# Kernel tuning notes

Hardware: AMD Instinct MI355X
Metric: run time of the kernel (lower is better)

## Reference

```python
import jax, jax.numpy as jnp
import numpy as np

TEMP = 10.0  # self.temp in the module


def _l2norm(x, eps):
    # matches torch cosine_similarity / F.normalize eps-clamped L2 normalization
    n = jnp.sqrt(jnp.sum(x * x, axis=-1, keepdims=True))
    return x / jnp.maximum(n, eps)


def setup_inputs() -> dict:
    key = jax.random.key(0)
    k1, k2, k3, k4 = jax.random.split(key, 4)
    b, n, k, q, t, c = 2, 5, 5, 75, 196, 384  # 5-way 5-shot, 15 queries/way, ViT-S tokens
    return {
        "feat_shot": jax.random.normal(k1, (b, n, k, t, c), jnp.float32),
        "feat_query": jax.random.normal(k2, (b, q, t, c), jnp.float32),
        "x_shot": jax.random.normal(k3, (b, n, k, c), jnp.float32),
        "x_query": jax.random.normal(k4, (b, q, c), jnp.float32),
    }


def reference(feat_shot, feat_query, x_shot, x_query):
    b, n, k, t, c = feat_shot.shape
    # --- token-level cosine similarity branch ---
    fq = _l2norm(feat_query, 1e-8)                      # [b,q,t,c]
    fs = _l2norm(feat_shot.reshape(b, n, k * t, c), 1e-8)  # [b,n,k*t,c]
    # cosine sim of every query token vs every shot token of each class
    sim = jnp.einsum('bqtc,bnsc->bqnts', fq, fs)        # [b,q,n,t,k*t]
    # topk(k=1) over shot tokens -> max; .mean(-1) over the size-1 topk dim is identity;
    # then mean over query tokens t
    logits = jnp.max(sim, axis=-1).mean(axis=-1)        # [b,q,n]
    # --- global-feature classifier branch ---
    proto = _l2norm(x_shot.mean(axis=-2), 1e-12)        # prototype mean over k shots: [b,n,c]
    xq = _l2norm(x_query, 1e-12)                        # [b,q,c]
    cls_logits = TEMP * jnp.einsum('bqc,bnc->bqn', xq, proto)  # [b,q,n]
    return (logits, cls_logits)
```

## Files before the change

### kernel.cpp

```cpp
#include <hip/hip_runtime.h>
#include <hip/hip_bf16.h>
#include <hip/hip_fp8.h>
#include <stdint.h>


typedef __attribute__((ext_vector_type(8))) int int8v;
typedef __attribute__((ext_vector_type(4))) float f32x4;

__device__ __forceinline__ unsigned enc_f(float f) {
    unsigned b = __float_as_uint(f);
    return (b & 0x80000000u) ? ~b : (b | 0x80000000u);
}
__device__ __forceinline__ float dec_f(unsigned u) {
    unsigned b = (u & 0x80000000u) ? (u & 0x7FFFFFFFu) : ~u;
    return __uint_as_float(b);
}

__device__ __forceinline__ unsigned pack4_fp8(float a, float b, float c, float d) {
    int r = __builtin_amdgcn_cvt_pk_fp8_f32(a, b, 0, false);
    r = __builtin_amdgcn_cvt_pk_fp8_f32(c, d, r, true);
    return (unsigned)r;
}

__global__ void prep_kernel(const float* __restrict__ feat_query,
                            const float* __restrict__ feat_shot,
                            const float* __restrict__ x_shot,
                            unsigned* __restrict__ fqn,
                            unsigned* __restrict__ fsnp,
                            float* __restrict__ proto,
                            unsigned* __restrict__ P) {
    const int blk  = blockIdx.x;
    const int tid  = threadIdx.x;
    const int lane = tid & 63;
    const int wv   = tid >> 6;

    if (blk < 2478) {
        const int tr  = blk * 16 + wv * 4 + (lane >> 4);
        const int l16 = lane & 15;
        if (tr >= 39640) return;

        const float* row;
        unsigned* o32;
        bool zero = false;
        if (tr < 29400) {
            row = feat_query + (size_t)tr * 384;
            o32 = fqn + (size_t)tr * 96;
        } else {
            const int sp = tr - 29400;
            const int bn = sp >> 10;
            const int s  = sp & 1023;
            o32 = fsnp + (size_t)sp * 96;
            row = feat_shot + ((size_t)bn * 980 + s) * 384;
            zero = (s >= 980);
        }
        if (zero) {
#pragma unroll
            for (int j = 0; j < 6; ++j) o32[l16 + 16 * j] = 0u;
            return;
        }
        const float4* rf4 = (const float4*)row;
        float4 v[6];
        float ss = 0.f;
#pragma unroll
        for (int j = 0; j < 6; ++j) {
            v[j] = rf4[l16 + 16 * j];
            ss += v[j].x * v[j].x + v[j].y * v[j].y + v[j].z * v[j].z + v[j].w * v[j].w;
        }
#pragma unroll
        for (int off = 1; off < 16; off <<= 1) ss += __shfl_xor(ss, off, 64);
        const float sc = 1.0f / fmaxf(sqrtf(ss), 1e-8f);
#pragma unroll
        for (int j = 0; j < 6; ++j)
            o32[l16 + 16 * j] = pack4_fp8(v[j].x * sc, v[j].y * sc, v[j].z * sc, v[j].w * sc);
    } else if (blk < 2481) {
        const int gw = (blk - 2478) * 4 + wv;
        if (gw >= 10) return;
        const float* base = x_shot + (size_t)gw * 5 * 384;
        float v[6];
        float ss = 0.f;
#pragma unroll
        for (int j = 0; j < 6; ++j) {
            float s = 0.f;
#pragma unroll
            for (int kk = 0; kk < 5; ++kk) s += base[kk * 384 + lane + 64 * j];
            s *= 0.2f;
            v[j] = s;
            ss += s * s;
        }
#pragma unroll
        for (int off = 1; off < 64; off <<= 1) ss += __shfl_xor(ss, off, 64);
        const float scale = 1.0f / fmaxf(sqrtf(ss), 1e-12f);
#pragma unroll
        for (int j = 0; j < 6; ++j) proto[(size_t)gw * 384 + lane + 64 * j] = v[j] * scale;
    } else {
        const int i = (blk - 2481) * 256 + tid;
        if (i < 147000) P[i] = 0u;
    }
}

__global__ __launch_bounds__(256, 2) void gemm_kernel(const uint8_t* __restrict__ fqn,
                                                      const uint8_t* __restrict__ fsnp,
                                                      unsigned* __restrict__ P) {
    __shared__ __align__(16) uint8_t Bl[2][12288];

    const int bid = blockIdx.x;
    const int mt  = bid % 58;
    const int g1  = bid / 58;
    const int sh  = g1 & 1;
    const int bc  = g1 >> 1;
    const int b   = bc / 5;
    const int m0  = mt * 256;

    const int tid  = threadIdx.x;
    const int lane = tid & 63;
    const int wv   = tid >> 6;
    const int l15  = lane & 15;
    const int hi   = lane >> 4;

    const uint8_t* Ag = fqn  + (size_t)b * 14700 * 384;
    const uint8_t* Bg = fsnp + ((size_t)bc * 1024 + sh * 512) * 384;

    int8v A[4][3];
#pragma unroll
    for (int mi = 0; mi < 4; ++mi) {
        int row = m0 + wv * 64 + mi * 16 + l15;
        row = row < 14700 ? row : 14699;
        const uint8_t* pa = Ag + (size_t)row * 384 + hi * 32;
#pragma unroll
        for (int ks = 0; ks < 3; ++ks) {
            const uint4 x = *(const uint4*)(pa + ks * 128);
            const uint4 y = *(const uint4*)(pa + ks * 128 + 16);
            A[mi][ks] = (int8v){(int)x.x, (int)x.y, (int)x.z, (int)x.w,
                                (int)y.x, (int)y.y, (int)y.z, (int)y.w};
        }
    }

    int src_off[3];
#pragma unroll
    for (int rr = 0; rr < 3; ++rr) {
        const int idx = rr * 256 + tid;
        const int col = idx / 24;
        const int gp  = idx - col * 24;
        const int g   = (gp & ~7) | ((gp & 7) ^ (col & 7));
        src_off[rr] = col * 384 + g * 16;
    }
    const int lds_base = tid * 16;

    uint4 nx0 = *(const uint4*)(Bg + src_off[0]);
    uint4 nx1 = *(const uint4*)(Bg + src_off[1]);
    uint4 nx2 = *(const uint4*)(Bg + src_off[2]);

    float rmax[4][4];
#pragma unroll
    for (int mi = 0; mi < 4; ++mi)
#pragma unroll
        for (int i = 0; i < 4; ++i) rmax[mi][i] = -3.0e38f;

    const int c0 = ((2 * hi + 0) ^ (l15 & 7)) * 16;
    const int c1 = ((2 * hi + 1) ^ (l15 & 7)) * 16;

    for (int it = 0; it < 16; ++it) {
        uint8_t* wbuf = Bl[it & 1];
        *(uint4*)(&wbuf[lds_base])        = nx0;
        *(uint4*)(&wbuf[lds_base + 4096]) = nx1;
        *(uint4*)(&wbuf[lds_base + 8192]) = nx2;
        __syncthreads();

        if (it + 1 < 16) {
            const uint8_t* src = Bg + (size_t)(it + 1) * 32 * 384;
            nx0 = *(const uint4*)(src + src_off[0]);
            nx1 = *(const uint4*)(src + src_off[1]);
            nx2 = *(const uint4*)(src + src_off[2]);
        }

        const uint8_t* buf = Bl[it & 1];
        f32x4 acc[4][2];
#pragma unroll
        for (int mi = 0; mi < 4; ++mi)
#pragma unroll
            for (int nf = 0; nf < 2; ++nf) acc[mi][nf] = (f32x4){0.f, 0.f, 0.f, 0.f};

#pragma unroll
        for (int ks = 0; ks < 3; ++ks) {
            int8v Bf[2];
#pragma unroll
            for (int nf = 0; nf < 2; ++nf) {
                const uint8_t* base = buf + (nf * 16 + l15) * 384 + ks * 128;
                const uint4 x = *(const uint4*)(base + c0);
                const uint4 y = *(const uint4*)(base + c1);
                Bf[nf] = (int8v){(int)x.x, (int)x.y, (int)x.z, (int)x.w,
                                 (int)y.x, (int)y.y, (int)y.z, (int)y.w};
            }
#pragma unroll
            for (int mi = 0; mi < 4; ++mi)
#pragma unroll
                for (int nf = 0; nf < 2; ++nf)
                    acc[mi][nf] = __builtin_amdgcn_mfma_scale_f32_16x16x128_f8f6f4(
                        A[mi][ks], Bf[nf], acc[mi][nf],
                        0, 0,
                        0, 0x7F7F7F7F,
                        0, 0x7F7F7F7F);
        }

#pragma unroll
        for (int nf = 0; nf < 2; ++nf) {
            if (sh * 512 + it * 32 + nf * 16 + l15 < 980) {
#pragma unroll
                for (int mi = 0; mi < 4; ++mi)
#pragma unroll
                    for (int i = 0; i < 4; ++i)
                        rmax[mi][i] = fmaxf(rmax[mi][i], acc[mi][nf][i]);
            }
        }
    }

#pragma unroll
    for (int mi = 0; mi < 4; ++mi)
#pragma unroll
        for (int i = 0; i < 4; ++i) {
            float v = rmax[mi][i];
#pragma unroll
            for (int off = 1; off < 16; off <<= 1) v = fmaxf(v, __shfl_xor(v, off, 64));
            if (l15 == 0) {
                const int row = m0 + wv * 64 + mi * 16 + hi * 4 + i;
                if (row < 14700)
                    atomicMax(&P[(size_t)bc * 14700 + row], enc_f(v));
            }
        }
}

__global__ void final_kernel(const unsigned* __restrict__ P,
                             const float* __restrict__ xq,
                             const float* __restrict__ proto,
                             float* __restrict__ out) {
    const int blk  = blockIdx.x;
    const int tid  = threadIdx.x;
    const int lane = tid & 63;
    const int wv   = tid >> 6;

    if (blk < 188) {
        const int gw = blk * 4 + wv;
        if (gw >= 750) return;
        const int n  = gw % 5;
        const int bq = gw / 5;
        const int b  = bq / 75;
        const int q  = bq % 75;
        const unsigned* row = P + (size_t)(b * 5 + n) * 14700 + q * 196;
        float s = 0.f;
        for (int t = lane; t < 196; t += 64) s += dec_f(row[t]);
#pragma unroll
        for (int off = 1; off < 64; off <<= 1) s += __shfl_xor(s, off, 64);
        if (lane == 0) out[gw] = s * (1.0f / 196.0f);
    } else {
        const int gw = (blk - 188) * 4 + wv;
        if (gw >= 150) return;
        const float* row = xq + (size_t)gw * 384;
        float u[6];
        float ss = 0.f;
#pragma unroll
        for (int j = 0; j < 6; ++j) { u[j] = row[lane + 64 * j]; ss += u[j] * u[j]; }
#pragma unroll
        for (int off = 1; off < 64; off <<= 1) ss += __shfl_xor(ss, off, 64);
        const float scale = 1.0f / fmaxf(sqrtf(ss), 1e-12f);
#pragma unroll
        for (int j = 0; j < 6; ++j) u[j] *= scale;
        const int b = gw / 75;
        for (int n = 0; n < 5; ++n) {
            const float* p = proto + (size_t)(b * 5 + n) * 384;
            float d = 0.f;
#pragma unroll
            for (int j = 0; j < 6; ++j) d += u[j] * p[lane + 64 * j];
#pragma unroll
            for (int off = 1; off < 64; off <<= 1) d += __shfl_xor(d, off, 64);
            if (lane == 0) out[750 + gw * 5 + n] = 10.0f * d;
        }
    }
}

extern "C" void kernel_launch(void* const* d_in, const int* in_sizes, int n_in,
                              void* d_out, int out_size, void* d_ws, size_t ws_size,
                              hipStream_t stream) {
    const float* feat_shot  = (const float*)d_in[0];
    const float* feat_query = (const float*)d_in[1];
    const float* x_shot     = (const float*)d_in[2];
    const float* x_query    = (const float*)d_in[3];
    float* out = (float*)d_out;
    char* ws = (char*)d_ws;

    uint8_t*  fqn   = (uint8_t*)ws;
    uint8_t*  fsnp  = (uint8_t*)(ws + 11289600);
    float*    proto = (float*)(ws + 15221760);
    unsigned* P     = (unsigned*)(ws + 15237120);

    prep_kernel<<<3056, 256, 0, stream>>>(feat_query, feat_shot, x_shot,
                                          (unsigned*)fqn, (unsigned*)fsnp, proto, P);
    gemm_kernel<<<1160, 256, 0, stream>>>(fqn, fsnp, P);
    final_kernel<<<226, 256, 0, stream>>>(P, x_query, proto, out);
}
```

Baseline: 157.0 us.

## Stream B tiles directly into LDS with async global_load_lds triple buffering

Replaces the register-staged B-tile loads and LDS stores with direct global-to-LDS async loads (global_load_lds, 16 bytes per lane), using three LDS buffers and manual vmcnt waits plus a raw s_barrier instead of __syncthreads. This removes the VGPR round trip and the LDS write instructions, and lets the next tile's load overlap compute. LDS use grows to 36KB per block, which may limit occupancy. The manual waitcnt and the barrier placement must be exactly right for the third buffer to stay race-free.

```diff
diff --git a/kernel.cpp b/kernel.cpp
--- a/kernel.cpp
+++ b/kernel.cpp
@@ -20,6 +20,12 @@
     int r = __builtin_amdgcn_cvt_pk_fp8_f32(a, b, 0, false);
     r = __builtin_amdgcn_cvt_pk_fp8_f32(c, d, r, true);
     return (unsigned)r;
+}
+
+__device__ __forceinline__ void gload_lds16(const uint8_t* g, uint8_t* l) {
+    __builtin_amdgcn_global_load_lds((const __attribute__((address_space(1))) void*)g,
+                                     (__attribute__((address_space(3))) void*)l,
+                                     16, 0, 0);
 }
 
 __global__ void prep_kernel(const float* __restrict__ feat_query,
@@ -101,7 +107,7 @@
 __global__ __launch_bounds__(256, 2) void gemm_kernel(const uint8_t* __restrict__ fqn,
                                                       const uint8_t* __restrict__ fsnp,
                                                       unsigned* __restrict__ P) {
-    __shared__ __align__(16) uint8_t Bl[2][12288];
+    __shared__ __align__(16) uint8_t Bl[3][12288];
 
     const int bid = blockIdx.x;
     const int mt  = bid % 58;
@@ -144,11 +150,10 @@
         const int g   = (gp & ~7) | ((gp & 7) ^ (col & 7));
         src_off[rr] = col * 384 + g * 16;
     }
-    const int lds_base = tid * 16;
-
-    uint4 nx0 = *(const uint4*)(Bg + src_off[0]);
-    uint4 nx1 = *(const uint4*)(Bg + src_off[1]);
-    uint4 nx2 = *(const uint4*)(Bg + src_off[2]);
+
+#pragma unroll
+    for (int rr = 0; rr < 3; ++rr)
+        gload_lds16(Bg + src_off[rr], &Bl[0][rr * 4096 + wv * 1024]);
 
     float rmax[4][4];
 #pragma unroll
@@ -159,21 +164,23 @@
     const int c0 = ((2 * hi + 0) ^ (l15 & 7)) * 16;
     const int c1 = ((2 * hi + 1) ^ (l15 & 7)) * 16;
 
+    int cur = 0;
     for (int it = 0; it < 16; ++it) {
-        uint8_t* wbuf = Bl[it & 1];
-        *(uint4*)(&wbuf[lds_base])        = nx0;
-        *(uint4*)(&wbuf[lds_base + 4096]) = nx1;
-        *(uint4*)(&wbuf[lds_base + 8192]) = nx2;
-        __syncthreads();
+        const int nxt = (cur == 2) ? 0 : cur + 1;
 
         if (it + 1 < 16) {
-            const uint8_t* src = Bg + (size_t)(it + 1) * 32 * 384;
-            nx0 = *(const uint4*)(src + src_off[0]);
-            nx1 = *(const uint4*)(src + src_off[1]);
-            nx2 = *(const uint4*)(src + src_off[2]);
-        }
-
-        const uint8_t* buf = Bl[it & 1];
+            const uint8_t* src = Bg + (size_t)(it + 1) * 12288;
+#pragma unroll
+            for (int rr = 0; rr < 3; ++rr)
+                gload_lds16(src + src_off[rr], &Bl[nxt][rr * 4096 + wv * 1024]);
+            asm volatile("s_waitcnt vmcnt(3)" ::: "memory");
+        } else {
+            asm volatile("s_waitcnt vmcnt(0)" ::: "memory");
+        }
+        __builtin_amdgcn_s_barrier();
+        asm volatile("" ::: "memory");
+
+        const uint8_t* buf = Bl[cur];
         f32x4 acc[4][2];
 #pragma unroll
         for (int mi = 0; mi < 4; ++mi)
@@ -212,6 +219,7 @@
                         rmax[mi][i] = fmaxf(rmax[mi][i], acc[mi][nf][i]);
             }
         }
+        cur = nxt;
     }
 
 #pragma unroll
```

Measured after the change: 161.9 us. +3.1%, slower.

## Pre-swizzle shot features into MFMA fragment layout and drop LDS staging

Applied to the files above, without the earlier changes.

The prep kernel now writes the normalized FP8 shot tokens in a layout that matches the MFMA B-fragment order, so each lane can load its operand straight from global memory with contiguous 16-byte loads. The GEMM kernel no longer stages B tiles through double-buffered shared memory with __syncthreads, and instead software-prefetches the next k-slice into registers. This removes LDS traffic and block-level barriers. The cost is that every wave loads B redundantly from global/L2 instead of sharing it through LDS, and the prefetch distance is shorter.

```diff
diff --git a/kernel.cpp b/kernel.cpp
--- a/kernel.cpp
+++ b/kernel.cpp
@@ -42,6 +42,7 @@
         const float* row;
         unsigned* o32;
         bool zero = false;
+        bool shot = false;
         if (tr < 29400) {
             row = feat_query + (size_t)tr * 384;
             o32 = fqn + (size_t)tr * 96;
@@ -49,13 +50,26 @@
             const int sp = tr - 29400;
             const int bn = sp >> 10;
             const int s  = sp & 1023;
-            o32 = fsnp + (size_t)sp * 96;
-            row = feat_shot + ((size_t)bn * 980 + s) * 384;
+            row  = feat_shot + ((size_t)bn * 980 + s) * 384;
             zero = (s >= 980);
-        }
+            shot = true;
+            const int shh   = s >> 9;
+            const int c     = s & 511;
+            const int chunk = c >> 5;
+            const int cl    = c & 31;
+            o32 = fsnp + (size_t)bn * 98304 + shh * 49152 + chunk * 3072
+                       + (cl >> 4) * 512 + (cl & 15) * 4;
+        }
+        int idxs[6];
+#pragma unroll
+        for (int j = 0; j < 6; ++j)
+            idxs[j] = shot ? ((j >> 1) * 1024 + ((l16 >> 2) & 1) * 256
+                              + (((j & 1) << 1) + (l16 >> 3)) * 64 + (l16 & 3))
+                           : (l16 + 16 * j);
+
         if (zero) {
 #pragma unroll
-            for (int j = 0; j < 6; ++j) o32[l16 + 16 * j] = 0u;
+            for (int j = 0; j < 6; ++j) o32[idxs[j]] = 0u;
             return;
         }
         const float4* rf4 = (const float4*)row;
@@ -71,7 +85,7 @@
         const float sc = 1.0f / fmaxf(sqrtf(ss), 1e-8f);
 #pragma unroll
         for (int j = 0; j < 6; ++j)
-            o32[l16 + 16 * j] = pack4_fp8(v[j].x * sc, v[j].y * sc, v[j].z * sc, v[j].w * sc);
+            o32[idxs[j]] = pack4_fp8(v[j].x * sc, v[j].y * sc, v[j].z * sc, v[j].w * sc);
     } else if (blk < 2481) {
         const int gw = (blk - 2478) * 4 + wv;
         if (gw >= 10) return;
@@ -101,8 +115,6 @@
 __global__ __launch_bounds__(256, 2) void gemm_kernel(const uint8_t* __restrict__ fqn,
                                                       const uint8_t* __restrict__ fsnp,
                                                       unsigned* __restrict__ P) {
-    __shared__ __align__(16) uint8_t Bl[2][12288];
-
     const int bid = blockIdx.x;
     const int mt  = bid % 58;
     const int g1  = bid / 58;
@@ -118,7 +130,8 @@
     const int hi   = lane >> 4;
 
     const uint8_t* Ag = fqn  + (size_t)b * 14700 * 384;
-    const uint8_t* Bg = fsnp + ((size_t)bc * 1024 + sh * 512) * 384;
+    const uint8_t* Bg = fsnp + (size_t)bc * 393216 + (size_t)sh * 196608;
+    const uint8_t* bp = Bg + lane * 16;
 
     int8v A[4][3];
 #pragma unroll
@@ -135,45 +148,18 @@
         }
     }
 
-    int src_off[3];
-#pragma unroll
-    for (int rr = 0; rr < 3; ++rr) {
-        const int idx = rr * 256 + tid;
-        const int col = idx / 24;
-        const int gp  = idx - col * 24;
-        const int g   = (gp & ~7) | ((gp & 7) ^ (col & 7));
-        src_off[rr] = col * 384 + g * 16;
-    }
-    const int lds_base = tid * 16;
-
-    uint4 nx0 = *(const uint4*)(Bg + src_off[0]);
-    uint4 nx1 = *(const uint4*)(Bg + src_off[1]);
-    uint4 nx2 = *(const uint4*)(Bg + src_off[2]);
-
     float rmax[4][4];
 #pragma unroll
     for (int mi = 0; mi < 4; ++mi)
 #pragma unroll
         for (int i = 0; i < 4; ++i) rmax[mi][i] = -3.0e38f;
 
-    const int c0 = ((2 * hi + 0) ^ (l15 & 7)) * 16;
-    const int c1 = ((2 * hi + 1) ^ (l15 & 7)) * 16;
-
-    for (int it = 0; it < 16; ++it) {
-        uint8_t* wbuf = Bl[it & 1];
-        *(uint4*)(&wbuf[lds_base])        = nx0;
-        *(uint4*)(&wbuf[lds_base + 4096]) = nx1;
-        *(uint4*)(&wbuf[lds_base + 8192]) = nx2;
-        __syncthreads();
-
-        if (it + 1 < 16) {
-            const uint8_t* src = Bg + (size_t)(it + 1) * 32 * 384;
-            nx0 = *(const uint4*)(src + src_off[0]);
-            nx1 = *(const uint4*)(src + src_off[1]);
-            nx2 = *(const uint4*)(src + src_off[2]);
-        }
-
-        const uint8_t* buf = Bl[it & 1];
+    uint4 nx0 = *(const uint4*)(bp);
+    uint4 ny0 = *(const uint4*)(bp + 1024);
+    uint4 nx1 = *(const uint4*)(bp + 2048);
+    uint4 ny1 = *(const uint4*)(bp + 3072);
+
+    for (int chunk = 0; chunk < 16; ++chunk) {
         f32x4 acc[4][2];
 #pragma unroll
         for (int mi = 0; mi < 4; ++mi)
@@ -182,29 +168,31 @@
 
 #pragma unroll
         for (int ks = 0; ks < 3; ++ks) {
-            int8v Bf[2];
-#pragma unroll
-            for (int nf = 0; nf < 2; ++nf) {
-                const uint8_t* base = buf + (nf * 16 + l15) * 384 + ks * 128;
-                const uint4 x = *(const uint4*)(base + c0);
-                const uint4 y = *(const uint4*)(base + c1);
-                Bf[nf] = (int8v){(int)x.x, (int)x.y, (int)x.z, (int)x.w,
-                                 (int)y.x, (int)y.y, (int)y.z, (int)y.w};
+            const int8v Bf0 = (int8v){(int)nx0.x, (int)nx0.y, (int)nx0.z, (int)nx0.w,
+                                      (int)ny0.x, (int)ny0.y, (int)ny0.z, (int)ny0.w};
+            const int8v Bf1 = (int8v){(int)nx1.x, (int)nx1.y, (int)nx1.z, (int)nx1.w,
+                                      (int)ny1.x, (int)ny1.y, (int)ny1.z, (int)ny1.w};
+            const int kk  = chunk * 3 + ks;
+            const int kkn = (kk + 1 < 48) ? kk + 1 : 47;
+            const uint8_t* p = bp + (size_t)kkn * 4096;
+            nx0 = *(const uint4*)(p);
+            ny0 = *(const uint4*)(p + 1024);
+            nx1 = *(const uint4*)(p + 2048);
+            ny1 = *(const uint4*)(p + 3072);
+#pragma unroll
+            for (int mi = 0; mi < 4; ++mi) {
+                acc[mi][0] = __builtin_amdgcn_mfma_scale_f32_16x16x128_f8f6f4(
+                    A[mi][ks], Bf0, acc[mi][0],
+                    0, 0, 0, 0x7F7F7F7F, 0, 0x7F7F7F7F);
+                acc[mi][1] = __builtin_amdgcn_mfma_scale_f32_16x16x128_f8f6f4(
+                    A[mi][ks], Bf1, acc[mi][1],
+                    0, 0, 0, 0x7F7F7F7F, 0, 0x7F7F7F7F);
             }
-#pragma unroll
-            for (int mi = 0; mi < 4; ++mi)
-#pragma unroll
-                for (int nf = 0; nf < 2; ++nf)
-                    acc[mi][nf] = __builtin_amdgcn_mfma_scale_f32_16x16x128_f8f6f4(
-                        A[mi][ks], Bf[nf], acc[mi][nf],
-                        0, 0,
-                        0, 0x7F7F7F7F,
-                        0, 0x7F7F7F7F);
         }
 
 #pragma unroll
         for (int nf = 0; nf < 2; ++nf) {
-            if (sh * 512 + it * 32 + nf * 16 + l15 < 980) {
+            if (sh * 512 + chunk * 32 + nf * 16 + l15 < 980) {
 #pragma unroll
                 for (int mi = 0; mi < 4; ++mi)
 #pragma unroll
```

Measured after the change: 167.9 us. 6.9% more time.
